# Kernel optimization log

Hardware: AMD Instinct MI355X
Metric: run time of the kernel (lower is better)

The kernel has to match this reference:

```python
import jax, jax.numpy as jnp
import numpy as np

B, L, D = 4, 4096, 1024
NEG_BIG = -1e30  # finite stand-in for log(0) to keep vjp NaN-free; exp underflows to 0


def log_g(x):
    # log of g(x) = where(x>=0, x+0.5, sigmoid(x)); log-space, branch-safe
    return jnp.where(x >= 0.0, jnp.log(jax.nn.relu(x) + 0.5), -jax.nn.softplus(-x))


def setup_inputs() -> dict:
    key = jax.random.key(0)
    ks = jax.random.split(key, 4)
    std = np.sqrt(2.0 / D)  # kaiming_normal for fan_in = D
    x = jax.random.normal(ks[0], (B, L, D), dtype=jnp.float32)
    W_f = jax.random.normal(ks[1], (D, D), dtype=jnp.float32) * std
    W_i = jax.random.normal(ks[2], (D, D), dtype=jnp.float32) * std
    W_h = jax.random.normal(ks[3], (D, D), dtype=jnp.float32) * std
    b_f = jnp.zeros((D,), dtype=jnp.float32)
    b_i = jnp.zeros((D,), dtype=jnp.float32)
    b_h = jnp.zeros((D,), dtype=jnp.float32)
    return {"x": x, "W_f": W_f, "b_f": b_f, "W_i": W_i, "b_i": b_i, "W_h": W_h, "b_h": b_h}


def reference(x, W_f, b_f, W_i, b_i, W_h, b_h):
    # gate pre-activations: (B, L, D)
    f_pre = jnp.einsum('bld,ed->ble', x, W_f) + b_f
    i_pre = jnp.einsum('bld,ed->ble', x, W_i) + b_i
    h_pre = jnp.einsum('bld,ed->ble', x, W_h) + b_h

    # log-space normalized gates: log_f + log_i parametrize f/(f+i), i/(f+i)
    diff = jax.nn.softplus(-f_pre) - jax.nn.softplus(-i_pre)
    log_f = -jax.nn.softplus(diff)
    log_i = -jax.nn.softplus(-diff)
    log_tilde_h = log_g(h_pre)

    b, l, d = x.shape
    log_h0 = jnp.full((b, 1, d), NEG_BIG, dtype=x.dtype)  # log(0)
    log_values = jnp.concatenate([log_h0, log_i + log_tilde_h], axis=1)  # (B, L+1, D)

    # associative parallel scan in log space
    a_star = jnp.pad(jnp.cumsum(log_f, axis=1), ((0, 0), (1, 0), (0, 0)))  # (B, L+1, D)
    log_h = a_star + jax.lax.cumlogsumexp(log_values - a_star, axis=1)
    return jnp.exp(log_h)[:, 1:]  # (B, L, D)
```

## Files before the change

kernel.cpp:

```cpp
#include <hip/hip_runtime.h>

#define M_TOTAL 16384
#define N_DIM   1024
#define K_DIM   1024
#define L_SEQ   4096
#define B_SZ    4
#define D_DIM   1024
#define CH      64
#define NCHUNK  (L_SEQ / CH)
#define NCHAN   (B_SZ * D_DIM)

#define BM 128
#define BN 128
#define BK 32
#define NKT (K_DIM / BK)
#define TPB 1024

typedef __attribute__((ext_vector_type(8))) short v8s;
typedef __attribute__((ext_vector_type(4))) float f32x4;

#define SB0()   __builtin_amdgcn_sched_barrier(0)
#define BAR()   __builtin_amdgcn_s_barrier()
#define WAITL0() do { asm volatile("s_waitcnt lgkmcnt(0)" ::: "memory"); SB0(); } while (0)
#define WAITV0() do { asm volatile("s_waitcnt vmcnt(0)"   ::: "memory"); SB0(); } while (0)
#define AS1 __attribute__((address_space(1)))
#define AS3 __attribute__((address_space(3)))

__device__ __forceinline__ ushort f2b(float f) {
  uint u = __float_as_uint(f);
  u += 0x7FFFu + ((u >> 16) & 1u);
  return (ushort)(u >> 16);
}
__device__ __forceinline__ float b2f(ushort u) {
  return __uint_as_float(((uint)u) << 16);
}

__global__ void cast_f32_bf16(const float* __restrict__ src, ushort* __restrict__ dst, int n4) {
  int i = blockIdx.x * blockDim.x + threadIdx.x;
  if (i >= n4) return;
  float4 v = reinterpret_cast<const float4*>(src)[i];
  ushort4 o = make_ushort4(f2b(v.x), f2b(v.y), f2b(v.z), f2b(v.w));
  reinterpret_cast<ushort4*>(dst)[i] = o;
}

__global__ void cast_w3(const float* __restrict__ s0, const float* __restrict__ s1,
                        const float* __restrict__ s2,
                        ushort* __restrict__ o0, ushort* __restrict__ o1, ushort* __restrict__ o2) {
  int i = blockIdx.x * blockDim.x + threadIdx.x;
  const float* s = (blockIdx.y == 0) ? s0 : (blockIdx.y == 1) ? s1 : s2;
  ushort* o      = (blockIdx.y == 0) ? o0 : (blockIdx.y == 1) ? o1 : o2;
  float4 v = reinterpret_cast<const float4*>(s)[i];
  ushort4 t = make_ushort4(f2b(v.x), f2b(v.y), f2b(v.z), f2b(v.w));
  reinterpret_cast<ushort4*>(o)[i] = t;
}

__device__ __forceinline__ void gates(float fp, float ip, float hp, float& a, float& v) {
  float Ef = __expf(-fp);
  float Ei = __expf(-ip);
  float r  = __builtin_amdgcn_rcpf(2.f + Ef + Ei);
  float f  = (1.f + Ei) * r;
  float i  = (1.f + Ef) * r;
  float ht = (hp >= 0.f) ? (hp + 0.5f) : __builtin_amdgcn_rcpf(1.f + __expf(-hp));
  a = f;
  v = i * ht;
}

__launch_bounds__(TPB, 4)
__global__ void gemm_fused(const ushort* __restrict__ X,
                           const ushort* __restrict__ W0, const ushort* __restrict__ W1,
                           const ushort* __restrict__ W2,
                           const float* __restrict__ bfp, const float* __restrict__ bip,
                           const float* __restrict__ bhp,
                           uint* __restrict__ Pav)
{
  __shared__ ushort lds[2][4][BM * BK];

  const int id = blockIdx.x;
  const int sw = (id & 7) * 128 + (id >> 3);
  const int n0 = (sw & 7) * BN;
  const int m0 = (sw >> 3) * BM;

  const int tid  = threadIdx.x;
  const int lane = tid & 63;
  const int w    = tid >> 6;
  const int wr   = w >> 3;
  const int wc   = w & 7;
  const int fr   = lane & 15, g = lane >> 4;

  int aoffh[4];
#pragma unroll
  for (int q = 0; q < 4; ++q) {
    int row = wr * 64 + q * 16 + fr;
    aoffh[q] = row * BK + ((g ^ ((row >> 1) & 3)) << 3);
  }
  const int rowB = wc * 16 + fr;
  const int boffh = rowB * BK + ((g ^ ((rowB >> 1) & 3)) << 3);

  const int id0 = tid, id1 = tid + TPB;
  const int mat0 = id0 >> 9, s0 = id0 & 511;
  const int mat1 = id1 >> 9, s1 = id1 & 511;
  const int r0 = s0 >> 2, k0 = (s0 & 3) ^ ((r0 >> 1) & 3);
  const int r1 = s1 >> 2, k1 = (s1 & 3) ^ ((r1 >> 1) & 3);
  const int dh0 = mat0 * (BM * BK) + s0 * 8;
  const int dh1 = mat1 * (BM * BK) + s1 * 8;

  const ushort* bases[4] = { X + (size_t)m0 * K_DIM, W0 + (size_t)n0 * K_DIM,
                             W1 + (size_t)n0 * K_DIM, W2 + (size_t)n0 * K_DIM };
  const ushort* g0 = bases[mat0] + (size_t)r0 * K_DIM + k0 * 8;
  const ushort* g1 = bases[mat1] + (size_t)r1 * K_DIM + k1 * 8;

  auto stage = [&](int buf, int kt) {
    __builtin_amdgcn_global_load_lds((const AS1 void*)(g0 + kt * BK),
        (AS3 void*)(&lds[buf][0][0] + dh0), 16, 0, 0);
    __builtin_amdgcn_global_load_lds((const AS1 void*)(g1 + kt * BK),
        (AS3 void*)(&lds[buf][0][0] + dh1), 16, 0, 0);
  };

  f32x4 acc[3][4] = {};

  stage(0, 0);
  WAITV0();
  BAR(); SB0();

  int cur = 0;
  for (int t = 0; t < NKT; ++t) {
    const bool pf = (t + 1 < NKT);
    const ushort* rb = &lds[cur][0][0];
    v8s aF[4], b0, b1, b2;
#pragma unroll
    for (int q = 0; q < 4; ++q)
      aF[q] = *reinterpret_cast<const v8s*>(rb + aoffh[q]);
    b0 = *reinterpret_cast<const v8s*>(rb + 1 * BM * BK + boffh);
    b1 = *reinterpret_cast<const v8s*>(rb + 2 * BM * BK + boffh);
    b2 = *reinterpret_cast<const v8s*>(rb + 3 * BM * BK + boffh);
    SB0();
    if (pf) stage(cur ^ 1, t + 1);
    SB0();
    WAITL0();
    __builtin_amdgcn_s_setprio(1);
#pragma unroll
    for (int mi = 0; mi < 4; ++mi) {
      acc[0][mi] = __builtin_amdgcn_mfma_f32_16x16x32_bf16(aF[mi], b0, acc[0][mi], 0, 0, 0);
      acc[1][mi] = __builtin_amdgcn_mfma_f32_16x16x32_bf16(aF[mi], b1, acc[1][mi], 0, 0, 0);
      acc[2][mi] = __builtin_amdgcn_mfma_f32_16x16x32_bf16(aF[mi], b2, acc[2][mi], 0, 0, 0);
    }
    __builtin_amdgcn_s_setprio(0);
    if (pf) {
      WAITV0();
      BAR(); SB0();
      cur ^= 1;
    }
  }

  const int col = n0 + wc * 16 + fr;
  const float vbf = bfp[col], vbi = bip[col], vbh = bhp[col];
#pragma unroll
  for (int mi = 0; mi < 4; ++mi) {
    const int row0 = m0 + wr * 64 + mi * 16 + g * 4;
#pragma unroll
    for (int r = 0; r < 4; ++r) {
      float a, v;
      gates(acc[0][mi][r] + vbf, acc[1][mi][r] + vbi, acc[2][mi][r] + vbh, a, v);
      Pav[(size_t)(row0 + r) * N_DIM + col] = (uint)f2b(a) | ((uint)f2b(v) << 16);
    }
  }
}

__global__ void scan_pass1(const uint4* __restrict__ Pav4,
                           float4* __restrict__ AggA, float4* __restrict__ AggV)
{
  int tid = blockIdx.x * blockDim.x + threadIdx.x;
  int c4 = tid & 1023;
  int chunk = tid >> 10;
  int b = c4 >> 8;
  int d4 = c4 & 255;
  size_t base4 = ((size_t)b * L_SEQ + (size_t)chunk * CH) * (D_DIM / 4) + d4;
  float A0 = 1.f, A1 = 1.f, A2 = 1.f, A3 = 1.f;
  float V0 = 0.f, V1 = 0.f, V2 = 0.f, V3 = 0.f;
#pragma unroll 4
  for (int t = 0; t < CH; ++t) {
    uint4 u = Pav4[base4 + (size_t)t * (D_DIM / 4)];
    float a0 = b2f((ushort)(u.x & 0xFFFFu)), v0 = b2f((ushort)(u.x >> 16));
    float a1 = b2f((ushort)(u.y & 0xFFFFu)), v1 = b2f((ushort)(u.y >> 16));
    float a2 = b2f((ushort)(u.z & 0xFFFFu)), v2 = b2f((ushort)(u.z >> 16));
    float a3 = b2f((ushort)(u.w & 0xFFFFu)), v3 = b2f((ushort)(u.w >> 16));
    A0 *= a0; V0 = fmaf(a0, V0, v0);
    A1 *= a1; V1 = fmaf(a1, V1, v1);
    A2 *= a2; V2 = fmaf(a2, V2, v2);
    A3 *= a3; V3 = fmaf(a3, V3, v3);
  }
  AggA[(size_t)chunk * (NCHAN / 4) + c4] = make_float4(A0, A1, A2, A3);
  AggV[(size_t)chunk * (NCHAN / 4) + c4] = make_float4(V0, V1, V2, V3);
}

__global__ void scan_mid(const float4* __restrict__ AggA, const float4* __restrict__ AggV,
                         float4* __restrict__ Start)
{
  int c4 = blockIdx.x * blockDim.x + threadIdx.x;
  float4 h = make_float4(0.f, 0.f, 0.f, 0.f);
#pragma unroll
  for (int j = 0; j < NCHUNK; ++j) {
    float4 A = AggA[(size_t)j * (NCHAN / 4) + c4];
    float4 V = AggV[(size_t)j * (NCHAN / 4) + c4];
    Start[(size_t)j * (NCHAN / 4) + c4] = h;
    h.x = fmaf(A.x, h.x, V.x);
    h.y = fmaf(A.y, h.y, V.y);
    h.z = fmaf(A.z, h.z, V.z);
    h.w = fmaf(A.w, h.w, V.w);
  }
}

__global__ void scan_pass2(const uint4* __restrict__ Pav4,
                           const float4* __restrict__ Start, float4* __restrict__ out4)
{
  int tid = blockIdx.x * blockDim.x + threadIdx.x;
  int c4 = tid & 1023;
  int chunk = tid >> 10;
  int b = c4 >> 8;
  int d4 = c4 & 255;
  size_t base4 = ((size_t)b * L_SEQ + (size_t)chunk * CH) * (D_DIM / 4) + d4;
  float4 h = Start[(size_t)chunk * (NCHAN / 4) + c4];
#pragma unroll 4
  for (int t = 0; t < CH; ++t) {
    size_t idx = base4 + (size_t)t * (D_DIM / 4);
    uint4 u = Pav4[idx];
    h.x = fmaf(b2f((ushort)(u.x & 0xFFFFu)), h.x, b2f((ushort)(u.x >> 16)));
    h.y = fmaf(b2f((ushort)(u.y & 0xFFFFu)), h.y, b2f((ushort)(u.y >> 16)));
    h.z = fmaf(b2f((ushort)(u.z & 0xFFFFu)), h.z, b2f((ushort)(u.z >> 16)));
    h.w = fmaf(b2f((ushort)(u.w & 0xFFFFu)), h.w, b2f((ushort)(u.w >> 16)));
    out4[idx] = h;
  }
}

extern "C" void kernel_launch(void* const* d_in, const int* in_sizes, int n_in,
                              void* d_out, int out_size, void* d_ws, size_t ws_size,
                              hipStream_t stream) {
  (void)in_sizes; (void)n_in; (void)out_size; (void)ws_size;
  const float* x  = (const float*)d_in[0];
  const float* Wf = (const float*)d_in[1];
  const float* bf = (const float*)d_in[2];
  const float* Wi = (const float*)d_in[3];
  const float* bi = (const float*)d_in[4];
  const float* Wh = (const float*)d_in[5];
  const float* bh = (const float*)d_in[6];

  ushort* xb  = (ushort*)d_ws;
  ushort* wfb = xb  + (size_t)M_TOTAL * K_DIM;
  ushort* wib = wfb + (size_t)N_DIM * K_DIM;
  ushort* whb = wib + (size_t)N_DIM * K_DIM;
  uint*  Pav  = (uint*)(whb + (size_t)N_DIM * K_DIM);
  float* AggA  = (float*)(Pav + (size_t)M_TOTAL * N_DIM);
  float* AggV  = AggA + NCHAN * NCHUNK;
  float* Start = AggV + NCHAN * NCHUNK;

  cast_f32_bf16<<<(M_TOTAL * K_DIM / 4) / 256, 256, 0, stream>>>(x, xb, M_TOTAL * K_DIM / 4);
  cast_w3<<<dim3((N_DIM * K_DIM / 4) / 256, 3), 256, 0, stream>>>(Wf, Wi, Wh, wfb, wib, whb);

  gemm_fused<<<dim3((M_TOTAL / BM) * (N_DIM / BN)), TPB, 0, stream>>>(
      xb, wfb, wib, whb, bf, bi, bh, Pav);

  scan_pass1<<<(NCHAN / 4 * NCHUNK) / 256, 256, 0, stream>>>(
      (const uint4*)Pav, (float4*)AggA, (float4*)AggV);
  scan_mid<<<(NCHAN / 4) / 256, 256, 0, stream>>>(
      (const float4*)AggA, (const float4*)AggV, (float4*)Start);
  scan_pass2<<<(NCHAN / 4 * NCHUNK) / 256, 256, 0, stream>>>(
      (const uint4*)Pav, (const float4*)Start, (float4*)d_out);
}
```

Baseline: 187.1 us.

## Load weight fragments directly into registers and shrink GEMM block to 512 threads

```diff
diff --git a/kernel.cpp b/kernel.cpp
--- a/kernel.cpp
+++ b/kernel.cpp
@@ -14,7 +14,7 @@
 #define BN 128
 #define BK 32
 #define NKT (K_DIM / BK)
-#define TPB 1024
+#define TPB 512
 
 typedef __attribute__((ext_vector_type(8))) short v8s;
 typedef __attribute__((ext_vector_type(4))) float f32x4;
@@ -65,7 +65,9 @@
   v = i * ht;
 }
 
-__launch_bounds__(TPB, 4)
+struct Bset { v8s m[3][2]; };
+
+__launch_bounds__(TPB, 2)
 __global__ void gemm_fused(const ushort* __restrict__ X,
                            const ushort* __restrict__ W0, const ushort* __restrict__ W1,
                            const ushort* __restrict__ W2,
@@ -73,18 +75,18 @@
                            const float* __restrict__ bhp,
                            uint* __restrict__ Pav)
 {
-  __shared__ ushort lds[2][4][BM * BK];
-
-  const int id = blockIdx.x;
-  const int sw = (id & 7) * 128 + (id >> 3);
-  const int n0 = (sw & 7) * BN;
-  const int m0 = (sw >> 3) * BM;
+  __shared__ ushort lds[2][BM * BK];
+
+  const int id  = blockIdx.x;
+  const int xcd = id & 7, j = id >> 3;
+  const int m0 = (xcd * 16 + (j & 15)) * BM;
+  const int n0 = (j >> 4) * BN;
 
   const int tid  = threadIdx.x;
   const int lane = tid & 63;
   const int w    = tid >> 6;
-  const int wr   = w >> 3;
-  const int wc   = w & 7;
+  const int wr   = w >> 2;
+  const int wc   = w & 3;
   const int fr   = lane & 15, g = lane >> 4;
 
   int aoffh[4];
@@ -93,75 +95,89 @@
     int row = wr * 64 + q * 16 + fr;
     aoffh[q] = row * BK + ((g ^ ((row >> 1) & 3)) << 3);
   }
-  const int rowB = wc * 16 + fr;
-  const int boffh = rowB * BK + ((g ^ ((rowB >> 1) & 3)) << 3);
-
-  const int id0 = tid, id1 = tid + TPB;
-  const int mat0 = id0 >> 9, s0 = id0 & 511;
-  const int mat1 = id1 >> 9, s1 = id1 & 511;
-  const int r0 = s0 >> 2, k0 = (s0 & 3) ^ ((r0 >> 1) & 3);
-  const int r1 = s1 >> 2, k1 = (s1 & 3) ^ ((r1 >> 1) & 3);
-  const int dh0 = mat0 * (BM * BK) + s0 * 8;
-  const int dh1 = mat1 * (BM * BK) + s1 * 8;
-
-  const ushort* bases[4] = { X + (size_t)m0 * K_DIM, W0 + (size_t)n0 * K_DIM,
-                             W1 + (size_t)n0 * K_DIM, W2 + (size_t)n0 * K_DIM };
-  const ushort* g0 = bases[mat0] + (size_t)r0 * K_DIM + k0 * 8;
-  const ushort* g1 = bases[mat1] + (size_t)r1 * K_DIM + k1 * 8;
-
-  auto stage = [&](int buf, int kt) {
-    __builtin_amdgcn_global_load_lds((const AS1 void*)(g0 + kt * BK),
-        (AS3 void*)(&lds[buf][0][0] + dh0), 16, 0, 0);
-    __builtin_amdgcn_global_load_lds((const AS1 void*)(g1 + kt * BK),
-        (AS3 void*)(&lds[buf][0][0] + dh1), 16, 0, 0);
+
+  const int r0 = tid >> 2;
+  const int k16 = (tid & 3) ^ ((r0 >> 1) & 3);
+  const ushort* gA = X + (size_t)(m0 + r0) * K_DIM + k16 * 8;
+  const int dh = tid * 8;
+
+  auto stageA = [&](int buf, int kt) {
+    __builtin_amdgcn_global_load_lds((const AS1 void*)(gA + kt * BK),
+        (AS3 void*)(&lds[buf][0] + dh), 16, 0, 0);
   };
 
-  f32x4 acc[3][4] = {};
-
-  stage(0, 0);
+  const int colb0 = n0 + wc * 32 + fr;
+  const ushort* pB[3][2];
+  pB[0][0] = W0 + (size_t)colb0 * K_DIM + g * 8;
+  pB[0][1] = W0 + (size_t)(colb0 + 16) * K_DIM + g * 8;
+  pB[1][0] = W1 + (size_t)colb0 * K_DIM + g * 8;
+  pB[1][1] = W1 + (size_t)(colb0 + 16) * K_DIM + g * 8;
+  pB[2][0] = W2 + (size_t)colb0 * K_DIM + g * 8;
+  pB[2][1] = W2 + (size_t)(colb0 + 16) * K_DIM + g * 8;
+
+  f32x4 acc[3][4][2] = {};
+  Bset BA, BB;
+
+#define LOADB(dst, kt)                                                        \
+  do {                                                                        \
+    _Pragma("unroll")                                                         \
+    for (int z = 0; z < 3; ++z)                                               \
+      _Pragma("unroll")                                                       \
+      for (int ni = 0; ni < 2; ++ni)                                          \
+        dst.m[z][ni] = *reinterpret_cast<const v8s*>(pB[z][ni] + (kt) * BK);  \
+  } while (0)
+
+  stageA(0, 0);
+  LOADB(BA, 0);
   WAITV0();
   BAR(); SB0();
 
-  int cur = 0;
-  for (int t = 0; t < NKT; ++t) {
-    const bool pf = (t + 1 < NKT);
-    const ushort* rb = &lds[cur][0][0];
-    v8s aF[4], b0, b1, b2;
-#pragma unroll
-    for (int q = 0; q < 4; ++q)
-      aF[q] = *reinterpret_cast<const v8s*>(rb + aoffh[q]);
-    b0 = *reinterpret_cast<const v8s*>(rb + 1 * BM * BK + boffh);
-    b1 = *reinterpret_cast<const v8s*>(rb + 2 * BM * BK + boffh);
-    b2 = *reinterpret_cast<const v8s*>(rb + 3 * BM * BK + boffh);
-    SB0();
-    if (pf) stage(cur ^ 1, t + 1);
-    SB0();
-    WAITL0();
-    __builtin_amdgcn_s_setprio(1);
+#define TILE_BODY(bcur, bnext, t)                                             \
+  do {                                                                        \
+    const bool pf = ((t) + 1 < NKT);                                          \
+    const int cur = (t) & 1;                                                  \
+    if (pf) { LOADB(bnext, (t) + 1); stageA(cur ^ 1, (t) + 1); }              \
+    SB0();                                                                    \
+    v8s aF[4];                                                                \
+    _Pragma("unroll")                                                         \
+    for (int q = 0; q < 4; ++q)                                               \
+      aF[q] = *reinterpret_cast<const v8s*>(&lds[cur][0] + aoffh[q]);         \
+    SB0();                                                                    \
+    WAITL0();                                                                 \
+    __builtin_amdgcn_s_setprio(1);                                            \
+    _Pragma("unroll")                                                         \
+    for (int z = 0; z < 3; ++z)                                               \
+      _Pragma("unroll")                                                       \
+      for (int mi = 0; mi < 4; ++mi) {                                        \
+        acc[z][mi][0] = __builtin_amdgcn_mfma_f32_16x16x32_bf16(              \
+            aF[mi], bcur.m[z][0], acc[z][mi][0], 0, 0, 0);                    \
+        acc[z][mi][1] = __builtin_amdgcn_mfma_f32_16x16x32_bf16(              \
+            aF[mi], bcur.m[z][1], acc[z][mi][1], 0, 0, 0);                    \
+      }                                                                       \
+    __builtin_amdgcn_s_setprio(0);                                            \
+    if (pf) { WAITV0(); BAR(); SB0(); }                                       \
+  } while (0)
+
+  for (int t = 0; t < NKT; t += 2) {
+    TILE_BODY(BA, BB, t);
+    TILE_BODY(BB, BA, t + 1);
+  }
+#undef TILE_BODY
+#undef LOADB
+
+#pragma unroll
+  for (int ni = 0; ni < 2; ++ni) {
+    const int col = n0 + wc * 32 + ni * 16 + fr;
+    const float vbf = bfp[col], vbi = bip[col], vbh = bhp[col];
 #pragma unroll
     for (int mi = 0; mi < 4; ++mi) {
-      acc[0][mi] = __builtin_amdgcn_mfma_f32_16x16x32_bf16(aF[mi], b0, acc[0][mi], 0, 0, 0);
-      acc[1][mi] = __builtin_amdgcn_mfma_f32_16x16x32_bf16(aF[mi], b1, acc[1][mi], 0, 0, 0);
-      acc[2][mi] = __builtin_amdgcn_mfma_f32_16x16x32_bf16(aF[mi], b2, acc[2][mi], 0, 0, 0);
-    }
-    __builtin_amdgcn_s_setprio(0);
-    if (pf) {
-      WAITV0();
-      BAR(); SB0();
-      cur ^= 1;
-    }
-  }
-
-  const int col = n0 + wc * 16 + fr;
-  const float vbf = bfp[col], vbi = bip[col], vbh = bhp[col];
-#pragma unroll
-  for (int mi = 0; mi < 4; ++mi) {
-    const int row0 = m0 + wr * 64 + mi * 16 + g * 4;
-#pragma unroll
-    for (int r = 0; r < 4; ++r) {
-      float a, v;
-      gates(acc[0][mi][r] + vbf, acc[1][mi][r] + vbi, acc[2][mi][r] + vbh, a, v);
-      Pav[(size_t)(row0 + r) * N_DIM + col] = (uint)f2b(a) | ((uint)f2b(v) << 16);
+      const int row0 = m0 + wr * 64 + mi * 16 + g * 4;
+#pragma unroll
+      for (int r = 0; r < 4; ++r) {
+        float a, v;
+        gates(acc[0][mi][ni][r] + vbf, acc[1][mi][ni][r] + vbi, acc[2][mi][ni][r] + vbh, a, v);
+        Pav[(size_t)(row0 + r) * N_DIM + col] = (uint)f2b(a) | ((uint)f2b(v) << 16);
+      }
     }
   }
 }
```

Result: slower. 296.7 us (+58.5%).

## Use 256x256 per-gate GEMM tiles and move gate math into scan passes

Applied to the files above, without the earlier changes.

```diff
diff --git a/kernel.cpp b/kernel.cpp
--- a/kernel.cpp
+++ b/kernel.cpp
@@ -10,11 +10,11 @@
 #define NCHUNK  (L_SEQ / CH)
 #define NCHAN   (B_SZ * D_DIM)
 
-#define BM 128
-#define BN 128
-#define BK 32
-#define NKT (K_DIM / BK)
-#define TPB 1024
+#define BM2 256
+#define BN2 256
+#define BK2 32
+#define NT  (K_DIM / BK2)
+#define GTPB 512
 
 typedef __attribute__((ext_vector_type(8))) short v8s;
 typedef __attribute__((ext_vector_type(4))) float f32x4;
@@ -22,6 +22,7 @@
 #define SB0()   __builtin_amdgcn_sched_barrier(0)
 #define BAR()   __builtin_amdgcn_s_barrier()
 #define WAITL0() do { asm volatile("s_waitcnt lgkmcnt(0)" ::: "memory"); SB0(); } while (0)
+#define WAITV4() do { asm volatile("s_waitcnt vmcnt(4)"   ::: "memory"); SB0(); } while (0)
 #define WAITV0() do { asm volatile("s_waitcnt vmcnt(0)"   ::: "memory"); SB0(); } while (0)
 #define AS1 __attribute__((address_space(1)))
 #define AS3 __attribute__((address_space(3)))
@@ -65,129 +66,152 @@
   v = i * ht;
 }
 
-__launch_bounds__(TPB, 4)
-__global__ void gemm_fused(const ushort* __restrict__ X,
-                           const ushort* __restrict__ W0, const ushort* __restrict__ W1,
-                           const ushort* __restrict__ W2,
-                           const float* __restrict__ bfp, const float* __restrict__ bip,
-                           const float* __restrict__ bhp,
-                           uint* __restrict__ Pav)
+__launch_bounds__(GTPB, 2)
+__global__ void gemm256(const ushort* __restrict__ X,
+                        const ushort* __restrict__ W0, const ushort* __restrict__ W1,
+                        const ushort* __restrict__ W2,
+                        const float* __restrict__ bfp, const float* __restrict__ bip,
+                        const float* __restrict__ bhp,
+                        ushort* __restrict__ P0, ushort* __restrict__ P1, ushort* __restrict__ P2)
 {
-  __shared__ ushort lds[2][4][BM * BK];
-
-  const int id = blockIdx.x;
-  const int sw = (id & 7) * 128 + (id >> 3);
-  const int n0 = (sw & 7) * BN;
-  const int m0 = (sw >> 3) * BM;
+  __shared__ ushort lds[4][16384];
+
+  const int q  = blockIdx.x;
+  const int wg = (q & 7) * 96 + (q >> 3);
+  const int z  = wg >> 8;
+  const int r_ = wg & 255;
+  const int n0 = (r_ >> 6) * BN2;
+  const int m0 = (r_ & 63) * BM2;
+
+  const ushort* W = (z == 0) ? W0 : (z == 1) ? W1 : W2;
+  ushort*       P = (z == 0) ? P0 : (z == 1) ? P1 : P2;
+  const float*  bias = (z == 0) ? bfp : (z == 1) ? bip : bhp;
 
   const int tid  = threadIdx.x;
   const int lane = tid & 63;
   const int w    = tid >> 6;
-  const int wr   = w >> 3;
-  const int wc   = w & 7;
+  const int wr   = w >> 2;
+  const int wc   = w & 3;
   const int fr   = lane & 15, g = lane >> 4;
 
-  int aoffh[4];
-#pragma unroll
-  for (int q = 0; q < 4; ++q) {
-    int row = wr * 64 + q * 16 + fr;
-    aoffh[q] = row * BK + ((g ^ ((row >> 1) & 3)) << 3);
-  }
-  const int rowB = wc * 16 + fr;
-  const int boffh = rowB * BK + ((g ^ ((rowB >> 1) & 3)) << 3);
-
-  const int id0 = tid, id1 = tid + TPB;
-  const int mat0 = id0 >> 9, s0 = id0 & 511;
-  const int mat1 = id1 >> 9, s1 = id1 & 511;
-  const int r0 = s0 >> 2, k0 = (s0 & 3) ^ ((r0 >> 1) & 3);
-  const int r1 = s1 >> 2, k1 = (s1 & 3) ^ ((r1 >> 1) & 3);
-  const int dh0 = mat0 * (BM * BK) + s0 * 8;
-  const int dh1 = mat1 * (BM * BK) + s1 * 8;
-
-  const ushort* bases[4] = { X + (size_t)m0 * K_DIM, W0 + (size_t)n0 * K_DIM,
-                             W1 + (size_t)n0 * K_DIM, W2 + (size_t)n0 * K_DIM };
-  const ushort* g0 = bases[mat0] + (size_t)r0 * K_DIM + k0 * 8;
-  const ushort* g1 = bases[mat1] + (size_t)r1 * K_DIM + k1 * 8;
-
-  auto stage = [&](int buf, int kt) {
-    __builtin_amdgcn_global_load_lds((const AS1 void*)(g0 + kt * BK),
-        (AS3 void*)(&lds[buf][0][0] + dh0), 16, 0, 0);
-    __builtin_amdgcn_global_load_lds((const AS1 void*)(g1 + kt * BK),
-        (AS3 void*)(&lds[buf][0][0] + dh1), 16, 0, 0);
+  int aoffh[8], boffh[4];
+#pragma unroll
+  for (int m = 0; m < 8; ++m) {
+    int row = wr * 128 + m * 16 + fr;
+    aoffh[m] = row * 32 + ((g ^ ((row >> 1) & 3)) << 3);
+  }
+#pragma unroll
+  for (int n = 0; n < 4; ++n) {
+    int row = wc * 64 + n * 16 + fr;
+    boffh[n] = 8192 + row * 32 + ((g ^ ((row >> 1) & 3)) << 3);
+  }
+
+  const int rA0 = tid >> 2,        qA0 = (tid & 3) ^ ((rA0 >> 1) & 3);
+  const int rA1 = 128 + (tid >> 2), qA1 = (tid & 3) ^ ((rA1 >> 1) & 3);
+  const ushort* gA0 = X + (size_t)(m0 + rA0) * K_DIM + qA0 * 8;
+  const ushort* gA1 = X + (size_t)(m0 + rA1) * K_DIM + qA1 * 8;
+  const ushort* gB0 = W + (size_t)(n0 + rA0) * K_DIM + qA0 * 8;
+  const ushort* gB1 = W + (size_t)(n0 + rA1) * K_DIM + qA1 * 8;
+  const int dh0 = tid * 8, dh1 = (512 + tid) * 8;
+
+  auto stageA = [&](int slot, int kt) {
+    __builtin_amdgcn_global_load_lds((const AS1 void*)(gA0 + kt * BK2),
+        (AS3 void*)(&lds[slot][dh0]), 16, 0, 0);
+    __builtin_amdgcn_global_load_lds((const AS1 void*)(gA1 + kt * BK2),
+        (AS3 void*)(&lds[slot][dh1]), 16, 0, 0);
   };
-
-  f32x4 acc[3][4] = {};
-
-  stage(0, 0);
-  WAITV0();
+  auto stageB = [&](int slot, int kt) {
+    __builtin_amdgcn_global_load_lds((const AS1 void*)(gB0 + kt * BK2),
+        (AS3 void*)(&lds[slot][8192 + dh0]), 16, 0, 0);
+    __builtin_amdgcn_global_load_lds((const AS1 void*)(gB1 + kt * BK2),
+        (AS3 void*)(&lds[slot][8192 + dh1]), 16, 0, 0);
+  };
+
+  f32x4 acc[8][4] = {};
+
+  stageA(0, 0); stageB(0, 0);
+  stageA(1, 1); stageB(1, 1);
+  WAITV4();
   BAR(); SB0();
 
-  int cur = 0;
-  for (int t = 0; t < NKT; ++t) {
-    const bool pf = (t + 1 < NKT);
-    const ushort* rb = &lds[cur][0][0];
-    v8s aF[4], b0, b1, b2;
-#pragma unroll
-    for (int q = 0; q < 4; ++q)
-      aF[q] = *reinterpret_cast<const v8s*>(rb + aoffh[q]);
-    b0 = *reinterpret_cast<const v8s*>(rb + 1 * BM * BK + boffh);
-    b1 = *reinterpret_cast<const v8s*>(rb + 2 * BM * BK + boffh);
-    b2 = *reinterpret_cast<const v8s*>(rb + 3 * BM * BK + boffh);
-    SB0();
-    if (pf) stage(cur ^ 1, t + 1);
-    SB0();
-    WAITL0();
+  for (int t = 0; t < NT; ++t) {
+    const int slot = t & 3;
+    const bool pf = (t + 2 < NT);
+    v8s aF[4], bF[4];
+
+#pragma unroll
+    for (int n = 0; n < 4; ++n) bF[n] = *reinterpret_cast<const v8s*>(&lds[slot][boffh[n]]);
+#pragma unroll
+    for (int m = 0; m < 4; ++m) aF[m] = *reinterpret_cast<const v8s*>(&lds[slot][aoffh[m]]);
+    if (pf) stageA((t + 2) & 3, t + 2);
+    SB0(); BAR(); WAITL0();
     __builtin_amdgcn_s_setprio(1);
 #pragma unroll
-    for (int mi = 0; mi < 4; ++mi) {
-      acc[0][mi] = __builtin_amdgcn_mfma_f32_16x16x32_bf16(aF[mi], b0, acc[0][mi], 0, 0, 0);
-      acc[1][mi] = __builtin_amdgcn_mfma_f32_16x16x32_bf16(aF[mi], b1, acc[1][mi], 0, 0, 0);
-      acc[2][mi] = __builtin_amdgcn_mfma_f32_16x16x32_bf16(aF[mi], b2, acc[2][mi], 0, 0, 0);
+    for (int m = 0; m < 4; ++m)
+#pragma unroll
+      for (int n = 0; n < 4; ++n)
+        acc[m][n] = __builtin_amdgcn_mfma_f32_16x16x32_bf16(aF[m], bF[n], acc[m][n], 0, 0, 0);
+    __builtin_amdgcn_s_setprio(0);
+    BAR(); SB0();
+
+#pragma unroll
+    for (int m = 0; m < 4; ++m) aF[m] = *reinterpret_cast<const v8s*>(&lds[slot][aoffh[4 + m]]);
+    if (pf) stageB((t + 2) & 3, t + 2);
+    SB0(); BAR(); WAITL0();
+    __builtin_amdgcn_s_setprio(1);
+#pragma unroll
+    for (int m = 0; m < 4; ++m)
+#pragma unroll
+      for (int n = 0; n < 4; ++n)
+        acc[4 + m][n] = __builtin_amdgcn_mfma_f32_16x16x32_bf16(aF[m], bF[n], acc[4 + m][n], 0, 0, 0);
+    __builtin_amdgcn_s_setprio(0);
+    if (t + 1 < NT) {
+      if (pf) { WAITV4(); } else { WAITV0(); }
+      BAR(); SB0();
     }
-    __builtin_amdgcn_s_setprio(0);
-    if (pf) {
-      WAITV0();
-      BAR(); SB0();
-      cur ^= 1;
+  }
+
+#pragma unroll
+  for (int m = 0; m < 8; ++m) {
+    const int row0 = m0 + wr * 128 + m * 16 + g * 4;
+#pragma unroll
+    for (int n = 0; n < 4; ++n) {
+      const int col = n0 + wc * 64 + n * 16 + fr;
+      const float bv = bias[col];
+#pragma unroll
+      for (int r = 0; r < 4; ++r)
+        P[(size_t)(row0 + r) * N_DIM + col] = f2b(acc[m][n][r] + bv);
     }
   }
-
-  const int col = n0 + wc * 16 + fr;
-  const float vbf = bfp[col], vbi = bip[col], vbh = bhp[col];
-#pragma unroll
-  for (int mi = 0; mi < 4; ++mi) {
-    const int row0 = m0 + wr * 64 + mi * 16 + g * 4;
-#pragma unroll
-    for (int r = 0; r < 4; ++r) {
-      float a, v;
-      gates(acc[0][mi][r] + vbf, acc[1][mi][r] + vbi, acc[2][mi][r] + vbh, a, v);
-      Pav[(size_t)(row0 + r) * N_DIM + col] = (uint)f2b(a) | ((uint)f2b(v) << 16);
-    }
-  }
-}
-
-__global__ void scan_pass1(const uint4* __restrict__ Pav4,
-                           float4* __restrict__ AggA, float4* __restrict__ AggV)
+}
+
+__global__ void scan_pass1g(const ushort4* __restrict__ Pf4, const ushort4* __restrict__ Pi4,
+                            const ushort4* __restrict__ Ph4,
+                            const float* __restrict__ bfp, const float* __restrict__ bip,
+                            const float* __restrict__ bhp,
+                            float4* __restrict__ AggA, float4* __restrict__ AggV)
 {
   int tid = blockIdx.x * blockDim.x + threadIdx.x;
   int c4 = tid & 1023;
   int chunk = tid >> 10;
   int b = c4 >> 8;
   int d4 = c4 & 255;
-  size_t base4 = ((size_t)b * L_SEQ + (size_t)chunk * CH) * (D_DIM / 4) + d4;
+  int d0 = d4 * 4;
+  float bf0 = bfp[d0], bf1 = bfp[d0 + 1], bf2 = bfp[d0 + 2], bf3 = bfp[d0 + 3];
+  float bi0 = bip[d0], bi1 = bip[d0 + 1], bi2 = bip[d0 + 2], bi3 = bip[d0 + 3];
+  float bh0 = bhp[d0], bh1 = bhp[d0 + 1], bh2 = bhp[d0 + 2], bh3 = bhp[d0 + 3];
+  size_t base = ((size_t)b * L_SEQ + (size_t)chunk * CH) * 256 + d4;
   float A0 = 1.f, A1 = 1.f, A2 = 1.f, A3 = 1.f;
   float V0 = 0.f, V1 = 0.f, V2 = 0.f, V3 = 0.f;
-#pragma unroll 4
+#pragma unroll 2
   for (int t = 0; t < CH; ++t) {
-    uint4 u = Pav4[base4 + (size_t)t * (D_DIM / 4)];
-    float a0 = b2f((ushort)(u.x & 0xFFFFu)), v0 = b2f((ushort)(u.x >> 16));
-    float a1 = b2f((ushort)(u.y & 0xFFFFu)), v1 = b2f((ushort)(u.y >> 16));
-    float a2 = b2f((ushort)(u.z & 0xFFFFu)), v2 = b2f((ushort)(u.z >> 16));
-    float a3 = b2f((ushort)(u.w & 0xFFFFu)), v3 = b2f((ushort)(u.w >> 16));
-    A0 *= a0; V0 = fmaf(a0, V0, v0);
-    A1 *= a1; V1 = fmaf(a1, V1, v1);
-    A2 *= a2; V2 = fmaf(a2, V2, v2);
-    A3 *= a3; V3 = fmaf(a3, V3, v3);
+    size_t idx = base + (size_t)t * 256;
+    ushort4 uf = Pf4[idx], ui = Pi4[idx], uh = Ph4[idx];
+    float a, v;
+    gates(b2f(uf.x) + bf0, b2f(ui.x) + bi0, b2f(uh.x) + bh0, a, v); A0 *= a; V0 = fmaf(a, V0, v);
+    gates(b2f(uf.y) + bf1, b2f(ui.y) + bi1, b2f(uh.y) + bh1, a, v); A1 *= a; V1 = fmaf(a, V1, v);
+    gates(b2f(uf.z) + bf2, b2f(ui.z) + bi2, b2f(uh.z) + bh2, a, v); A2 *= a; V2 = fmaf(a, V2, v);
+    gates(b2f(uf.w) + bf3, b2f(ui.w) + bi3, b2f(uh.w) + bh3, a, v); A3 *= a; V3 = fmaf(a, V3, v);
   }
   AggA[(size_t)chunk * (NCHAN / 4) + c4] = make_float4(A0, A1, A2, A3);
   AggV[(size_t)chunk * (NCHAN / 4) + c4] = make_float4(V0, V1, V2, V3);
@@ -210,24 +234,32 @@
   }
 }
 
-__global__ void scan_pass2(const uint4* __restrict__ Pav4,
-                           const float4* __restrict__ Start, float4* __restrict__ out4)
+__global__ void scan_pass2g(const ushort4* __restrict__ Pf4, const ushort4* __restrict__ Pi4,
+                            const ushort4* __restrict__ Ph4,
+                            const float* __restrict__ bfp, const float* __restrict__ bip,
+                            const float* __restrict__ bhp,
+                            const float4* __restrict__ Start, float4* __restrict__ out4)
 {
   int tid = blockIdx.x * blockDim.x + threadIdx.x;
   int c4 = tid & 1023;
   int chunk = tid >> 10;
   int b = c4 >> 8;
   int d4 = c4 & 255;
-  size_t base4 = ((size_t)b * L_SEQ + (size_t)chunk * CH) * (D_DIM / 4) + d4;
+  int d0 = d4 * 4;
+  float bf0 = bfp[d0], bf1 = bfp[d0 + 1], bf2 = bfp[d0 + 2], bf3 = bfp[d0 + 3];
+  float bi0 = bip[d0], bi1 = bip[d0 + 1], bi2 = bip[d0 + 2], bi3 = bip[d0 + 3];
+  float bh0 = bhp[d0], bh1 = bhp[d0 + 1], bh2 = bhp[d0 + 2], bh3 = bhp[d0 + 3];
+  size_t base = ((size_t)b * L_SEQ + (size_t)chunk * CH) * 256 + d4;
   float4 h = Start[(size_t)chunk * (NCHAN / 4) + c4];
-#pragma unroll 4
+#pragma unroll 2
   for (int t = 0; t < CH; ++t) {
-    size_t idx = base4 + (size_t)t * (D_DIM / 4);
-    uint4 u = Pav4[idx];
-    h.x = fmaf(b2f((ushort)(u.x & 0xFFFFu)), h.x, b2f((ushort)(u.x >> 16)));
-    h.y = fmaf(b2f((ushort)(u.y & 0xFFFFu)), h.y, b2f((ushort)(u.y >> 16)));
-    h.z = fmaf(b2f((ushort)(u.z & 0xFFFFu)), h.z, b2f((ushort)(u.z >> 16)));
-    h.w = fmaf(b2f((ushort)(u.w & 0xFFFFu)), h.w, b2f((ushort)(u.w >> 16)));
+    size_t idx = base + (size_t)t * 256;
+    ushort4 uf = Pf4[idx], ui = Pi4[idx], uh = Ph4[idx];
+    float a, v;
+    gates(b2f(uf.x) + bf0, b2f(ui.x) + bi0, b2f(uh.x) + bh0, a, v); h.x = fmaf(a, h.x, v);
+    gates(b2f(uf.y) + bf1, b2f(ui.y) + bi1, b2f(uh.y) + bh1, a, v); h.y = fmaf(a, h.y, v);
+    gates(b2f(uf.z) + bf2, b2f(ui.z) + bi2, b2f(uh.z) + bh2, a, v); h.z = fmaf(a, h.z, v);
+    gates(b2f(uf.w) + bf3, b2f(ui.w) + bi3, b2f(uh.w) + bh3, a, v); h.w = fmaf(a, h.w, v);
     out4[idx] = h;
   }
 }
@@ -248,21 +280,25 @@
   ushort* wfb = xb  + (size_t)M_TOTAL * K_DIM;
   ushort* wib = wfb + (size_t)N_DIM * K_DIM;
   ushort* whb = wib + (size_t)N_DIM * K_DIM;
-  uint*  Pav  = (uint*)(whb + (size_t)N_DIM * K_DIM);
-  float* AggA  = (float*)(Pav + (size_t)M_TOTAL * N_DIM);
-  float* AggV  = AggA + NCHAN * NCHUNK;
-  float* Start = AggV + NCHAN * NCHUNK;
+  ushort* Pf  = whb + (size_t)N_DIM * K_DIM;
+  ushort* Pi  = Pf  + (size_t)M_TOTAL * N_DIM;
+  ushort* Ph  = Pi  + (size_t)M_TOTAL * N_DIM;
+  float*  AggA  = (float*)(Ph + (size_t)M_TOTAL * N_DIM);
+  float*  AggV  = AggA + NCHAN * NCHUNK;
+  float*  Start = AggV + NCHAN * NCHUNK;
 
   cast_f32_bf16<<<(M_TOTAL * K_DIM / 4) / 256, 256, 0, stream>>>(x, xb, M_TOTAL * K_DIM / 4);
   cast_w3<<<dim3((N_DIM * K_DIM / 4) / 256, 3), 256, 0, stream>>>(Wf, Wi, Wh, wfb, wib, whb);
 
-  gemm_fused<<<dim3((M_TOTAL / BM) * (N_DIM / BN)), TPB, 0, stream>>>(
-      xb, wfb, wib, whb, bf, bi, bh, Pav);
-
-  scan_pass1<<<(NCHAN / 4 * NCHUNK) / 256, 256, 0, stream>>>(
-      (const uint4*)Pav, (float4*)AggA, (float4*)AggV);
+  gemm256<<<dim3(3 * (M_TOTAL / BM2) * (N_DIM / BN2)), GTPB, 0, stream>>>(
+      xb, wfb, wib, whb, bf, bi, bh, Pf, Pi, Ph);
+
+  scan_pass1g<<<(NCHAN / 4 * NCHUNK) / 256, 256, 0, stream>>>(
+      (const ushort4*)Pf, (const ushort4*)Pi, (const ushort4*)Ph,
+      bf, bi, bh, (float4*)AggA, (float4*)AggV);
   scan_mid<<<(NCHAN / 4) / 256, 256, 0, stream>>>(
       (const float4*)AggA, (const float4*)AggV, (float4*)Start);
-  scan_pass2<<<(NCHAN / 4 * NCHUNK) / 256, 256, 0, stream>>>(
-      (const uint4*)Pav, (const float4*)Start, (float4*)d_out);
-}
+  scan_pass2g<<<(NCHAN / 4 * NCHUNK) / 256, 256, 0, stream>>>(
+      (const ushort4*)Pf, (const ushort4*)Pi, (const ushort4*)Ph,
+      bf, bi, bh, (const float4*)Start, (float4*)d_out);
+}
```

Measured after the change: 225.7 us. 20.6% more time.
